# Kernel optimization log

Hardware: AMD Instinct MI355X
Metric: run time of the kernel (lower is better)

The kernel has to match this reference:

```python
import jax, jax.numpy as jnp
import numpy as np

D = 384
H = 6
DK = D // H
EPS = 1e-5


def _layernorm(x, g, b):
    mu = jnp.mean(x, axis=-1, keepdims=True)
    var = jnp.var(x, axis=-1, keepdims=True)
    return (x - mu) * jax.lax.rsqrt(var + EPS) * g + b


def setup_inputs() -> dict:
    key = jax.random.key(0)
    ks = jax.random.split(key, 12)
    B, N = 8, 2048
    s = lambda fan_in: 1.0 / np.sqrt(fan_in)
    return {
        "points": jax.random.normal(ks[0], (B, 3 + D, N), dtype=jnp.float32),
        "ln1_g": jnp.ones((D,), jnp.float32),
        "ln1_b": jnp.zeros((D,), jnp.float32),
        "w_qkv": jax.random.uniform(ks[1], (3 * D, D), jnp.float32, -s(D), s(D)),
        "w_o": jax.random.uniform(ks[2], (D, D), jnp.float32, -s(D), s(D)),
        "b_o": jnp.zeros((D,), jnp.float32),
        "ln2_g": jnp.ones((D,), jnp.float32),
        "ln2_b": jnp.zeros((D,), jnp.float32),
        "w1": jax.random.uniform(ks[3], (2 * D, D), jnp.float32, -s(D), s(D)),
        "b1": jnp.zeros((2 * D,), jnp.float32),
        "w2": jax.random.uniform(ks[4], (D, 2 * D), jnp.float32, -s(2 * D), s(2 * D)),
        "b2": jnp.zeros((D,), jnp.float32),
    }


def reference(points, ln1_g, ln1_b, w_qkv, w_o, b_o, ln2_g, ln2_b, w1, b1, w2, b2):
    coords = points[:, :3, :]                       # [B, 3, N]
    feats = jnp.transpose(points[:, 3:, :], (0, 2, 1))  # [B, N, D]
    B, N, _ = feats.shape

    # pre-norm + fused QKV projection (no bias)
    h = _layernorm(feats, ln1_g, ln1_b)
    qkv = jnp.einsum('bnd,ed->bne', h, w_qkv)       # [B, N, 3D]
    q, k, v = jnp.split(qkv, 3, axis=-1)

    split_heads = lambda t: jnp.transpose(t.reshape(B, N, H, DK), (0, 2, 1, 3))
    q, k, v = split_heads(q), split_heads(k), split_heads(v)  # [B, H, N, DK]

    scale = DK ** -0.5
    scores = jnp.einsum('bhid,bhjd->bhij', q, k) * scale      # [B, H, N, N]
    attn = jax.nn.softmax(scores, axis=-1)
    ctx = jnp.einsum('bhij,bhjd->bhid', attn, v)              # [B, H, N, DK]
    ctx = jnp.transpose(ctx, (0, 2, 1, 3)).reshape(B, N, D)
    attn_out = jnp.einsum('bnd,ed->bne', ctx, w_o) + b_o

    x = feats + attn_out
    # FFN with exact (erf) GELU, hidden = 2*D
    h2 = _layernorm(x, ln2_g, ln2_b)
    ff = jnp.einsum('bnd,ed->bne', h2, w1) + b1
    ff = jax.nn.gelu(ff, approximate=False)
    ff = jnp.einsum('bne,de->bnd', ff, w2) + b2
    x = x + ff

    return jnp.concatenate([coords, jnp.transpose(x, (0, 2, 1))], axis=1)
```

## Files before the change

kernel.cpp:

```cpp
#include <hip/hip_runtime.h>
#include <cstdint>


typedef __bf16 bf16;
typedef __bf16 bf16x8 __attribute__((ext_vector_type(8)));
typedef __bf16 bf16x4 __attribute__((ext_vector_type(4)));
typedef float floatx4 __attribute__((ext_vector_type(4)));
typedef uint32_t __attribute__((address_space(1))) gu32;
typedef uint32_t __attribute__((address_space(3))) lu32;

#define NN 2048
#define DD 384
#define HH 6
#define DK 64
#define BB 8
#define MM (BB * NN)
#define D3 (3 * DD)
#define D2 (2 * DD)
#define CH (3 + DD)
#define LP 72

#define QSCALE 0.18033688011112042f


__global__ void cast_w_kernel(const float* __restrict__ in, bf16* __restrict__ out, int n) {
    int i = blockIdx.x * 256 + threadIdx.x;
    if (i < n) out[i] = (bf16)in[i];
}

__global__ void coords_kernel(const float* __restrict__ pts, float* __restrict__ out) {
    int i = blockIdx.x * 256 + threadIdx.x;
    int b = i / (3 * NN), r = i % (3 * NN);
    out[(size_t)b * CH * NN + r] = pts[(size_t)b * CH * NN + r];
}

__global__ void transpose_kernel(const float* __restrict__ pts, float* __restrict__ feats) {
    __shared__ float T[32][33];
    int n0 = blockIdx.x * 32, d0 = blockIdx.y * 32, b = blockIdx.z;
    int tx = threadIdx.x, ty = threadIdx.y;
    const float* src = pts + (size_t)b * CH * NN;
#pragma unroll
    for (int i = 0; i < 4; ++i)
        T[ty + i * 8][tx] = src[(size_t)(3 + d0 + ty + i * 8) * NN + n0 + tx];
    __syncthreads();
    float* dst = feats + (size_t)b * NN * DD;
#pragma unroll
    for (int i = 0; i < 4; ++i)
        dst[(size_t)(n0 + ty + i * 8) * DD + d0 + tx] = T[tx][ty + i * 8];
}

__global__ __launch_bounds__(256) void ln_kernel(const float* __restrict__ x,
                                                 const float* __restrict__ g,
                                                 const float* __restrict__ bta,
                                                 bf16* __restrict__ out) {
    int wave = threadIdx.x >> 6, lane = threadIdx.x & 63;
    int row = blockIdx.x * 4 + wave;
    const float* xr = x + (size_t)row * DD;
    float v[6], s = 0.f, sq = 0.f;
#pragma unroll
    for (int i = 0; i < 6; ++i) { v[i] = xr[lane + i * 64]; s += v[i]; sq += v[i] * v[i]; }
#pragma unroll
    for (int o = 1; o < 64; o <<= 1) { s += __shfl_xor(s, o); sq += __shfl_xor(sq, o); }
    float mu = s * (1.f / DD);
    float var = sq * (1.f / DD) - mu * mu;
    float rs = rsqrtf(var + 1e-5f);
    bf16* orow = out + (size_t)row * DD;
#pragma unroll
    for (int i = 0; i < 6; ++i) {
        int d = lane + i * 64;
        orow[d] = (bf16)((v[i] - mu) * rs * g[d] + bta[d]);
    }
}

template <int NC, int K, int MODE>
__global__ __launch_bounds__(256, 2)
void gemm_bt(const bf16* __restrict__ A, const bf16* __restrict__ W,
             const float* __restrict__ bias, const float* __restrict__ res,
             bf16* __restrict__ obf, float* __restrict__ of32, bf16* __restrict__ vt) {
    __shared__ bf16 As[128 * 32];
    __shared__ bf16 Ws[128 * 32];
    const int t = threadIdx.x;
    const int wave = t >> 6, lane = t & 63;
    const int m0 = blockIdx.x * 128, n0 = blockIdx.y * 128;
    const int wm = (wave >> 1) * 64, wn = (wave & 1) * 64;
    const int lr = lane & 15, quad = lane >> 4;
    const int sr = t >> 2, sc = (t & 3) * 8;

    floatx4 acc[4][4];
#pragma unroll
    for (int mi = 0; mi < 4; ++mi)
#pragma unroll
        for (int ni = 0; ni < 4; ++ni) {
            floatx4 z = {0.f, 0.f, 0.f, 0.f};
            acc[mi][ni] = z;
        }

    for (int k0 = 0; k0 < K; k0 += 32) {
        __syncthreads();
#pragma unroll
        for (int i = 0; i < 2; ++i) {
            const int r = i * 64 + sr;
            __builtin_amdgcn_global_load_lds(
                (const gu32*)&A[(size_t)(m0 + r) * K + k0 + sc],
                (lu32*)&As[r * 32 + sc], 16, 0, 0);
            __builtin_amdgcn_global_load_lds(
                (const gu32*)&W[(size_t)(n0 + r) * K + k0 + sc],
                (lu32*)&Ws[r * 32 + sc], 16, 0, 0);
        }
        __syncthreads();
        bf16x8 af[4], bfr[4];
#pragma unroll
        for (int mi = 0; mi < 4; ++mi)
            af[mi] = *(const bf16x8*)&As[(wm + mi * 16 + lr) * 32 + quad * 8];
#pragma unroll
        for (int ni = 0; ni < 4; ++ni)
            bfr[ni] = *(const bf16x8*)&Ws[(wn + ni * 16 + lr) * 32 + quad * 8];
#pragma unroll
        for (int mi = 0; mi < 4; ++mi)
#pragma unroll
            for (int ni = 0; ni < 4; ++ni)
                acc[mi][ni] = __builtin_amdgcn_mfma_f32_16x16x32_bf16(af[mi], bfr[ni], acc[mi][ni], 0, 0, 0);
    }

#pragma unroll
    for (int mi = 0; mi < 4; ++mi) {
#pragma unroll
        for (int ni = 0; ni < 4; ++ni) {
            const int r0 = m0 + wm + mi * 16 + quad * 4;
            const int c = n0 + wn + ni * 16 + lr;
            floatx4 v = acc[mi][ni];
            if constexpr (MODE == 0) {
                const int cb = n0 + wn + ni * 16;
                if (cb >= 2 * DD) {
                    const int hh = (c - 2 * DD) >> 6, dk = (c - 2 * DD) & 63;
                    const int b = r0 >> 11, n = r0 & (NN - 1);
                    bf16x4 pk;
#pragma unroll
                    for (int r = 0; r < 4; ++r) pk[r] = (bf16)v[r];
                    *(bf16x4*)&vt[((size_t)(b * HH + hh) * DK + dk) * NN + n] = pk;
                } else {
                    const float sc_q = (cb < DD) ? QSCALE : 1.0f;
#pragma unroll
                    for (int r = 0; r < 4; ++r) obf[(size_t)(r0 + r) * NC + c] = (bf16)(v[r] * sc_q);
                }
            } else if constexpr (MODE == 1) {
#pragma unroll
                for (int r = 0; r < 4; ++r)
                    of32[(size_t)(r0 + r) * NC + c] = v[r] + bias[c] + res[(size_t)(r0 + r) * NC + c];
            } else if constexpr (MODE == 2) {
#pragma unroll
                for (int r = 0; r < 4; ++r) {
                    float u = v[r] + bias[c];
                    obf[(size_t)(r0 + r) * NC + c] = (bf16)(0.5f * u * (1.f + erff(u * 0.70710678118f)));
                }
            } else {
                const int b = r0 >> 11, n = r0 & (NN - 1);
                float o4[4];
#pragma unroll
                for (int r = 0; r < 4; ++r)
                    o4[r] = v[r] + bias[c] + res[(size_t)(r0 + r) * DD + c];
                float4 val = make_float4(o4[0], o4[1], o4[2], o4[3]);
                *(float4*)&of32[((size_t)b * CH + 3 + c) * NN + n] = val;
            }
        }
    }
}

__global__ __launch_bounds__(256, 4)
void attn_kernel(const bf16* __restrict__ qkv, const bf16* __restrict__ vt,
                 bf16* __restrict__ ctx) {
    __shared__ bf16 Ks[64 * LP];
    __shared__ bf16 Vs[64 * LP];
    __shared__ bf16 Ps[4][32 * LP];
    const int t = threadIdx.x, wave = t >> 6, lane = t & 63;
    const int lr = lane & 15, quad = lane >> 4;
    const int bh = blockIdx.y, b = bh / HH, h = bh % HH;
    const int q0 = blockIdx.x * 128;
    const bf16* qbase = qkv + (size_t)b * NN * D3 + h * DK;
    const bf16* kbase = qbase + DD;
    const bf16* vbase = vt + (size_t)bh * DK * NN;

    bf16x8 aq[2][2];
#pragma unroll
    for (int mi = 0; mi < 2; ++mi)
#pragma unroll
        for (int ks = 0; ks < 2; ++ks)
            aq[mi][ks] = *(const bf16x8*)&qbase[(size_t)(q0 + wave * 32 + mi * 16 + lr) * D3 +
                                                ks * 32 + quad * 8];

    bf16x8 ones;
#pragma unroll
    for (int i = 0; i < 8; ++i) ones[i] = (bf16)1.0f;

    floatx4 o[2][4], ol[2];
#pragma unroll
    for (int mi = 0; mi < 2; ++mi) {
        floatx4 z = {0.f, 0.f, 0.f, 0.f};
        ol[mi] = z;
#pragma unroll
        for (int nd = 0; nd < 4; ++nd) o[mi][nd] = z;
    }

    for (int j0 = 0; j0 < NN; j0 += 64) {
        __syncthreads();
        {
            const int rr = t >> 3, cc = (t & 7) * 8;
#pragma unroll
            for (int i = 0; i < 2; ++i) {
                const int j = i * 32 + rr;
                *(bf16x8*)&Ks[j * LP + cc] =
                    *(const bf16x8*)&kbase[(size_t)(j0 + j) * D3 + cc];
                *(bf16x8*)&Vs[j * LP + cc] =
                    *(const bf16x8*)&vbase[(size_t)j * NN + j0 + cc];
            }
        }
        __syncthreads();

        floatx4 s[2][4];
#pragma unroll
        for (int mi = 0; mi < 2; ++mi)
#pragma unroll
            for (int nj = 0; nj < 4; ++nj) {
                floatx4 z = {0.f, 0.f, 0.f, 0.f};
                s[mi][nj] = z;
            }
#pragma unroll
        for (int ks = 0; ks < 2; ++ks)
#pragma unroll
            for (int nj = 0; nj < 4; ++nj) {
                bf16x8 bk = *(const bf16x8*)&Ks[(nj * 16 + lr) * LP + ks * 32 + quad * 8];
#pragma unroll
                for (int mi = 0; mi < 2; ++mi)
                    s[mi][nj] = __builtin_amdgcn_mfma_f32_16x16x32_bf16(bk, aq[mi][ks], s[mi][nj], 0, 0, 0);
            }

#pragma unroll
        for (int mi = 0; mi < 2; ++mi)
#pragma unroll
            for (int nj = 0; nj < 4; ++nj) {
                bf16x4 pk;
#pragma unroll
                for (int r = 0; r < 4; ++r) pk[r] = (bf16)exp2f(s[mi][nj][r]);
                *(bf16x4*)&Ps[wave][(mi * 16 + lr) * LP + nj * 16 + quad * 4] = pk;
            }

#pragma unroll
        for (int ks = 0; ks < 2; ++ks) {
            bf16x8 ap[2];
#pragma unroll
            for (int mi = 0; mi < 2; ++mi)
                ap[mi] = *(const bf16x8*)&Ps[wave][(mi * 16 + lr) * LP + ks * 32 + quad * 8];
#pragma unroll
            for (int nd = 0; nd < 4; ++nd) {
                bf16x8 bv = *(const bf16x8*)&Vs[(nd * 16 + lr) * LP + ks * 32 + quad * 8];
#pragma unroll
                for (int mi = 0; mi < 2; ++mi)
                    o[mi][nd] = __builtin_amdgcn_mfma_f32_16x16x32_bf16(ap[mi], bv, o[mi][nd], 0, 0, 0);
            }
#pragma unroll
            for (int mi = 0; mi < 2; ++mi)
                ol[mi] = __builtin_amdgcn_mfma_f32_16x16x32_bf16(ap[mi], ones, ol[mi], 0, 0, 0);
        }
    }

#pragma unroll
    for (int mi = 0; mi < 2; ++mi)
#pragma unroll
        for (int r = 0; r < 4; ++r) {
            const int n = q0 + wave * 32 + mi * 16 + quad * 4 + r;
            const float inv = 1.0f / ol[mi][r];
#pragma unroll
            for (int nd = 0; nd < 4; ++nd) {
                const int d = h * DK + nd * 16 + lr;
                ctx[(size_t)(b * NN + n) * DD + d] = (bf16)(o[mi][nd][r] * inv);
            }
        }
}


extern "C" void kernel_launch(void* const* d_in, const int* in_sizes, int n_in,
                              void* d_out, int out_size, void* d_ws, size_t ws_size,
                              hipStream_t stream) {
    const float* points = (const float*)d_in[0];
    const float* ln1_g = (const float*)d_in[1];
    const float* ln1_b = (const float*)d_in[2];
    const float* w_qkv = (const float*)d_in[3];
    const float* w_o   = (const float*)d_in[4];
    const float* b_o   = (const float*)d_in[5];
    const float* ln2_g = (const float*)d_in[6];
    const float* ln2_b = (const float*)d_in[7];
    const float* w1    = (const float*)d_in[8];
    const float* b1    = (const float*)d_in[9];
    const float* w2    = (const float*)d_in[10];
    const float* b2    = (const float*)d_in[11];
    float* out = (float*)d_out;

    char* ws = (char*)d_ws;
    size_t off = 0;
    auto alloc = [&](size_t bytes) -> void* {
        void* p = ws + off;
        off += (bytes + 255) & ~(size_t)255;
        return p;
    };
    float* feats = (float*)alloc((size_t)MM * DD * 4);
    float* xbuf  = (float*)alloc((size_t)MM * DD * 4);
    bf16* h1     = (bf16*)alloc((size_t)MM * DD * 2);
    bf16* h2     = (bf16*)alloc((size_t)MM * DD * 2);
    bf16* qkvb   = (bf16*)alloc((size_t)MM * D3 * 2);
    bf16* vtb    = (bf16*)alloc((size_t)BB * HH * DK * NN * 2);
    bf16* ctx    = (bf16*)alloc((size_t)MM * DD * 2);
    bf16* ffh    = (bf16*)alloc((size_t)MM * D2 * 2);
    bf16* wqkv_bf = (bf16*)alloc((size_t)D3 * DD * 2);
    bf16* wo_bf   = (bf16*)alloc((size_t)DD * DD * 2);
    bf16* w1_bf   = (bf16*)alloc((size_t)D2 * DD * 2);
    bf16* w2_bf   = (bf16*)alloc((size_t)DD * D2 * 2);

    cast_w_kernel<<<(D3 * DD + 255) / 256, 256, 0, stream>>>(w_qkv, wqkv_bf, D3 * DD);
    cast_w_kernel<<<(DD * DD + 255) / 256, 256, 0, stream>>>(w_o, wo_bf, DD * DD);
    cast_w_kernel<<<(D2 * DD + 255) / 256, 256, 0, stream>>>(w1, w1_bf, D2 * DD);
    cast_w_kernel<<<(DD * D2 + 255) / 256, 256, 0, stream>>>(w2, w2_bf, DD * D2);
    coords_kernel<<<(BB * 3 * NN) / 256, 256, 0, stream>>>(points, out);
    transpose_kernel<<<dim3(NN / 32, DD / 32, BB), dim3(32, 8), 0, stream>>>(points, feats);
    ln_kernel<<<MM / 4, 256, 0, stream>>>(feats, ln1_g, ln1_b, h1);
    gemm_bt<D3, DD, 0><<<dim3(MM / 128, D3 / 128), 256, 0, stream>>>(
        h1, wqkv_bf, nullptr, nullptr, qkvb, nullptr, vtb);
    attn_kernel<<<dim3(NN / 128, BB * HH), 256, 0, stream>>>(qkvb, vtb, ctx);
    gemm_bt<DD, DD, 1><<<dim3(MM / 128, DD / 128), 256, 0, stream>>>(
        ctx, wo_bf, b_o, feats, nullptr, xbuf, nullptr);
    ln_kernel<<<MM / 4, 256, 0, stream>>>(xbuf, ln2_g, ln2_b, h2);
    gemm_bt<D2, DD, 2><<<dim3(MM / 128, D2 / 128), 256, 0, stream>>>(
        h2, w1_bf, b1, nullptr, ffh, nullptr, nullptr);
    gemm_bt<DD, D2, 3><<<dim3(MM / 128, DD / 128), 256, 0, stream>>>(
        ffh, w2_bf, b2, xbuf, nullptr, out, nullptr);
}
```

Before: 308.5 us.

## Keep softmax probabilities in registers for PV MFMA and fuse weight casts

The attention kernel no longer writes exp'd scores to a per-wave LDS buffer and reads them back. Instead the S accumulator layout is fed straight into the 16x16x16 bf16 MFMA as the A operand, with V read as 4-element slices from LDS. This removes the LDS round trip and frees shared memory, but uses twice as many smaller MFMAs for PV and for the row-sum. Separately, the four weight-cast launches are merged into one kernel to cut launch overhead.

```diff
diff --git a/kernel.cpp b/kernel.cpp
--- a/kernel.cpp
+++ b/kernel.cpp
@@ -5,6 +5,7 @@
 typedef __bf16 bf16;
 typedef __bf16 bf16x8 __attribute__((ext_vector_type(8)));
 typedef __bf16 bf16x4 __attribute__((ext_vector_type(4)));
+typedef short s16x4 __attribute__((ext_vector_type(4)));
 typedef float floatx4 __attribute__((ext_vector_type(4)));
 typedef uint32_t __attribute__((address_space(1))) gu32;
 typedef uint32_t __attribute__((address_space(3))) lu32;
@@ -22,10 +23,20 @@
 
 #define QSCALE 0.18033688011112042f
 
-
-__global__ void cast_w_kernel(const float* __restrict__ in, bf16* __restrict__ out, int n) {
+static __device__ __forceinline__ s16x4 as_s16x4(bf16x4 v) {
+    union { bf16x4 b; s16x4 s; } u; u.b = v; return u.s;
+}
+
+
+__global__ void cast_all_kernel(const float* __restrict__ w_qkv, const float* __restrict__ w_o,
+                                const float* __restrict__ w1, const float* __restrict__ w2,
+                                bf16* __restrict__ o_qkv, bf16* __restrict__ o_o,
+                                bf16* __restrict__ o_w1, bf16* __restrict__ o_w2) {
     int i = blockIdx.x * 256 + threadIdx.x;
-    if (i < n) out[i] = (bf16)in[i];
+    if (i < 442368) o_qkv[i] = (bf16)w_qkv[i];
+    else if (i < 589824) o_o[i - 442368] = (bf16)w_o[i - 442368];
+    else if (i < 884736) o_w1[i - 589824] = (bf16)w1[i - 589824];
+    else o_w2[i - 884736] = (bf16)w2[i - 884736];
 }
 
 __global__ void coords_kernel(const float* __restrict__ pts, float* __restrict__ out) {
@@ -171,7 +182,6 @@
                  bf16* __restrict__ ctx) {
     __shared__ bf16 Ks[64 * LP];
     __shared__ bf16 Vs[64 * LP];
-    __shared__ bf16 Ps[4][32 * LP];
     const int t = threadIdx.x, wave = t >> 6, lane = t & 63;
     const int lr = lane & 15, quad = lane >> 4;
     const int bh = blockIdx.y, b = bh / HH, h = bh % HH;
@@ -188,9 +198,10 @@
             aq[mi][ks] = *(const bf16x8*)&qbase[(size_t)(q0 + wave * 32 + mi * 16 + lr) * D3 +
                                                 ks * 32 + quad * 8];
 
-    bf16x8 ones;
-#pragma unroll
-    for (int i = 0; i < 8; ++i) ones[i] = (bf16)1.0f;
+    bf16x4 ones4;
+#pragma unroll
+    for (int i = 0; i < 4; ++i) ones4[i] = (bf16)1.0f;
+    const s16x4 ones_s = as_s16x4(ones4);
 
     floatx4 o[2][4], ol[2];
 #pragma unroll
@@ -235,31 +246,25 @@
             }
 
 #pragma unroll
-        for (int mi = 0; mi < 2; ++mi)
-#pragma unroll
-            for (int nj = 0; nj < 4; ++nj) {
+        for (int nj = 0; nj < 4; ++nj) {
+            s16x4 ap[2];
+#pragma unroll
+            for (int mi = 0; mi < 2; ++mi) {
                 bf16x4 pk;
 #pragma unroll
                 for (int r = 0; r < 4; ++r) pk[r] = (bf16)exp2f(s[mi][nj][r]);
-                *(bf16x4*)&Ps[wave][(mi * 16 + lr) * LP + nj * 16 + quad * 4] = pk;
-            }
-
-#pragma unroll
-        for (int ks = 0; ks < 2; ++ks) {
-            bf16x8 ap[2];
+                ap[mi] = as_s16x4(pk);
+            }
+#pragma unroll
+            for (int nd = 0; nd < 4; ++nd) {
+                s16x4 bv = as_s16x4(*(const bf16x4*)&Vs[(nd * 16 + lr) * LP + nj * 16 + quad * 4]);
+#pragma unroll
+                for (int mi = 0; mi < 2; ++mi)
+                    o[mi][nd] = __builtin_amdgcn_mfma_f32_16x16x16bf16_1k(ap[mi], bv, o[mi][nd], 0, 0, 0);
+            }
 #pragma unroll
             for (int mi = 0; mi < 2; ++mi)
-                ap[mi] = *(const bf16x8*)&Ps[wave][(mi * 16 + lr) * LP + ks * 32 + quad * 8];
-#pragma unroll
-            for (int nd = 0; nd < 4; ++nd) {
-                bf16x8 bv = *(const bf16x8*)&Vs[(nd * 16 + lr) * LP + ks * 32 + quad * 8];
-#pragma unroll
-                for (int mi = 0; mi < 2; ++mi)
-                    o[mi][nd] = __builtin_amdgcn_mfma_f32_16x16x32_bf16(ap[mi], bv, o[mi][nd], 0, 0, 0);
-            }
-#pragma unroll
-            for (int mi = 0; mi < 2; ++mi)
-                ol[mi] = __builtin_amdgcn_mfma_f32_16x16x32_bf16(ap[mi], ones, ol[mi], 0, 0, 0);
+                ol[mi] = __builtin_amdgcn_mfma_f32_16x16x16bf16_1k(ap[mi], ones_s, ol[mi], 0, 0, 0);
         }
     }
 
@@ -315,10 +320,8 @@
     bf16* w1_bf   = (bf16*)alloc((size_t)D2 * DD * 2);
     bf16* w2_bf   = (bf16*)alloc((size_t)DD * D2 * 2);
 
-    cast_w_kernel<<<(D3 * DD + 255) / 256, 256, 0, stream>>>(w_qkv, wqkv_bf, D3 * DD);
-    cast_w_kernel<<<(DD * DD + 255) / 256, 256, 0, stream>>>(w_o, wo_bf, DD * DD);
-    cast_w_kernel<<<(D2 * DD + 255) / 256, 256, 0, stream>>>(w1, w1_bf, D2 * DD);
-    cast_w_kernel<<<(DD * D2 + 255) / 256, 256, 0, stream>>>(w2, w2_bf, DD * D2);
+    cast_all_kernel<<<1179648 / 256, 256, 0, stream>>>(w_qkv, w_o, w1, w2,
+                                                       wqkv_bf, wo_bf, w1_bf, w2_bf);
     coords_kernel<<<(BB * 3 * NN) / 256, 256, 0, stream>>>(points, out);
     transpose_kernel<<<dim3(NN / 32, DD / 32, BB), dim3(32, 8), 0, stream>>>(points, feats);
     ln_kernel<<<MM / 4, 256, 0, stream>>>(feats, ln1_g, ln1_b, h1);
```

Result: faster. 299.7 us (-2.8%).
